# Performance work log

Hardware: AMD Instinct MI355X
Metric: run time of the kernel (lower is better)

The kernel has to match this reference:

```python
import jax, jax.numpy as jnp
import numpy as np

T, B, D, L, C, H = 100, 4096, 32, 32, 64, 128  # steps, batch, state_dim, latent, context, hidden


def setup_inputs() -> dict:
    key = jax.random.key(0)
    ks = jax.random.split(key, 32)
    def rn(k, shape, scale=0.1):
        return jax.random.normal(k, shape, dtype=jnp.float32) * scale
    return dict(
        xs=rn(ks[0], (T, B, D), 1.0),
        ts=jnp.arange(T, dtype=jnp.float32) * 0.01,
        eps0=rn(ks[1], (B, L), 1.0),
        noise=rn(ks[2], (T - 1, B, L), 1.0),
        gru_Wih=rn(ks[3], (3 * H, D)), gru_Whh=rn(ks[4], (3 * H, H)),
        gru_bih=rn(ks[5], (3 * H,)), gru_bhh=rn(ks[6], (3 * H,)),
        enc_W=rn(ks[7], (C, H)), enc_b=rn(ks[8], (C,)),
        qz0_W=rn(ks[9], (2 * L, C)), qz0_b=rn(ks[10], (2 * L,)),
        fW1=rn(ks[11], (H, L + C)), fb1=rn(ks[12], (H,)),
        fW2=rn(ks[13], (H, H)), fb2=rn(ks[14], (H,)),
        fW3=rn(ks[15], (L, H)), fb3=rn(ks[16], (L,)),
        hW1=rn(ks[17], (H, L)), hb1=rn(ks[18], (H,)),
        hW2=rn(ks[19], (H, H)), hb2=rn(ks[20], (H,)),
        hW3=rn(ks[21], (L, H)), hb3=rn(ks[22], (L,)),
        gW1=rn(ks[23], (L, H)), gb1=rn(ks[24], (L, H)),
        gW2=rn(ks[25], (L, H)), gb2=rn(ks[26], (L,)),
        projW=rn(ks[27], (D, L)), projb=rn(ks[28], (D,)),
    )


def reference(xs, ts, eps0, noise, gru_Wih, gru_Whh, gru_bih, gru_bhh,
              enc_W, enc_b, qz0_W, qz0_b,
              fW1, fb1, fW2, fb2, fW3, fb3,
              hW1, hb1, hW2, hb2, hW3, hb3,
              gW1, gb1, gW2, gb2, projW, projb):
    sp = jax.nn.softplus

    # --- Encoder: GRU (PyTorch gate order r,z,n) + Linear ---
    def gru_step(h, x):
        gi = x @ gru_Wih.T + gru_bih
        gh = h @ gru_Whh.T + gru_bhh
        ir, iz, inn = jnp.split(gi, 3, axis=-1)
        hr, hz, hn = jnp.split(gh, 3, axis=-1)
        r = jax.nn.sigmoid(ir + hr)
        z = jax.nn.sigmoid(iz + hz)
        n = jnp.tanh(inn + r * hn)
        h = (1.0 - z) * n + z * h
        return h, h

    h0 = jnp.zeros((xs.shape[1], gru_Whh.shape[1]), xs.dtype)
    _, hs = jax.lax.scan(gru_step, h0, xs)          # [T,B,H]
    ctx = hs @ enc_W.T + enc_b                      # [T,B,C]

    # --- posterior z0 ---
    qz0 = ctx[0] @ qz0_W.T + qz0_b
    mean, logstd = jnp.split(qz0, 2, axis=-1)
    z0 = mean + jnp.exp(logstd) * eps0              # [B,L]

    def f_mlp(x):  # posterior drift f_net
        return sp(sp(x @ fW1.T + fb1) @ fW2.T + fb2) @ fW3.T + fb3

    def h_mlp(y):  # prior drift h_net
        return sp(sp(y @ hW1.T + hb1) @ hW2.T + hb2) @ hW3.T + hb3

    def diag_g(y):  # batched per-dim 1->H->1 sigmoid MLPs (the g_nets loop)
        hmid = sp(y[..., None] * gW1 + gb1)          # [B,L,H]
        return jax.nn.sigmoid(jnp.sum(hmid * gW2, -1) + gb2)  # [B,L]

    dts = ts[1:] - ts[:-1]

    def sde_step(carry, inp):
        y, lq = carry
        c, dt, dW = inp
        f = f_mlp(jnp.concatenate([y, c], axis=-1))
        hdr = h_mlp(y)
        g = diag_g(y)
        u = (f - hdr) / g                            # KL path-wise term
        lq = lq + 0.5 * jnp.sum(u * u, axis=-1) * dt
        y = y + f * dt + g * jnp.sqrt(dt) * dW       # Euler-Maruyama
        return (y, lq), y

    (zT, logqp), ys = jax.lax.scan(
        sde_step, (z0, jnp.zeros(z0.shape[0], z0.dtype)), (ctx[:-1], dts, noise))
    zs = jnp.concatenate([z0[None], ys], axis=0)     # [T,B,L]
    xs_hat = zs @ projW.T + projb                    # [T,B,D]
    return xs_hat, logqp
```

## Files before the change

### kernel.cpp

```cpp
#include <hip/hip_runtime.h>


#define TT 100
#define BB 4096
#define DD 32
#define LL 32
#define CC 64
#define HH 128
#define GROW 260

typedef _Float16 h1;
typedef _Float16 h2 __attribute__((ext_vector_type(2)));
typedef _Float16 f16x8 __attribute__((ext_vector_type(8)));
typedef float f32x4 __attribute__((ext_vector_type(4)));

#define MFMA(a, b, c) __builtin_amdgcn_mfma_f32_16x16x32_f16(a, b, c, 0, 0, 0)
#define PIN(x) asm volatile("" : "+v"(x))

__device__ __forceinline__ void bar_lds() {
  __builtin_amdgcn_sched_barrier(0);
  asm volatile("s_waitcnt lgkmcnt(0)" ::: "memory");
  __builtin_amdgcn_s_barrier();
  asm volatile("" ::: "memory");
  __builtin_amdgcn_sched_barrier(0);
}

__device__ __forceinline__ float sigm(float x) {
  return __frcp_rn(1.0f + __expf(-x));
}
__device__ __forceinline__ float tanh_(float x) {
  float e = __expf(2.0f * fminf(x, 15.0f));
  return (e - 1.0f) * __frcp_rn(e + 1.0f);
}
__device__ __forceinline__ float splus(float x) {
  return __logf(1.0f + __expf(x));
}

__device__ __forceinline__ f16x8 bfrag(const float* __restrict__ W, int K,
                                       int n0, int k0, int lane) {
  const float* p = W + (size_t)(n0 + (lane & 15)) * K + k0 + ((lane >> 4) << 3);
  f16x8 r;
#pragma unroll
  for (int j = 0; j < 8; ++j) r[j] = (h1)p[j];
  return r;
}

__device__ __forceinline__ f16x8 afrag(const h1* base, int ld, int k0,
                                       int lane) {
  return *(const f16x8*)(base + (size_t)(lane & 15) * ld + k0 +
                         ((lane >> 4) << 3));
}

__global__ __launch_bounds__(320) void k_gtab(
    const float* __restrict__ gW1, const float* __restrict__ gb1,
    const float* __restrict__ gW2, const float* __restrict__ gb2,
    float* __restrict__ gtab) {
  const int l = blockIdx.x;
  const int e = threadIdx.x;
  if (e >= 257) return;
  const float yv = -12.f + (float)e * (24.f / 256.f);
  const float* w1 = gW1 + l * HH;
  const float* bb = gb1 + l * HH;
  const float* w2 = gW2 + l * HH;
  float a = 0.f;
#pragma unroll 4
  for (int h = 0; h < HH; ++h)
    a = fmaf(splus(fmaf(yv, w1[h], bb[h])), w2[h], a);
  gtab[l * GROW + e] = sigm(a + gb2[l]);
}

__global__ __launch_bounds__(512, 2) void k_gru(
    const float* __restrict__ xs, const float* __restrict__ Wih,
    const float* __restrict__ Whh, const float* __restrict__ bih,
    const float* __restrict__ bhh, const float* __restrict__ encW,
    const float* __restrict__ encb, h1* __restrict__ ctx16) {
  __shared__ alignas(16) h1 sH[2][16][136];
  __shared__ alignas(16) h1 sX[2][16][40];

  const int tid = threadIdx.x;
  const int lane = tid & 63, w = tid >> 6;
  const int b0 = blockIdx.x * 16;
  const int coln = lane & 15, row4 = (lane >> 4) << 2;

  f16x8 wIH[3], wHH[3][4], wE[4];
#pragma unroll
  for (int g = 0; g < 3; ++g) {
    wIH[g] = bfrag(Wih, DD, 128 * g + 16 * w, 0, lane);
#pragma unroll
    for (int kt = 0; kt < 4; ++kt)
      wHH[g][kt] = bfrag(Whh, HH, 128 * g + 16 * w, 32 * kt, lane);
  }
  const int m = 16 * w + coln;
  const float b_r = bih[m] + bhh[m];
  const float b_z = bih[128 + m] + bhh[128 + m];
  const float b_ni = bih[256 + m];
  const float b_nh = bhh[256 + m];
  const int ccE = (w >= 4) ? 16 * (w - 4) + coln : 0;
  const float bE = (w >= 4) ? encb[ccE] : 0.f;
  if (w >= 4) {
#pragma unroll
    for (int kt = 0; kt < 4; ++kt)
      wE[kt] = bfrag(encW, HH, 16 * (w - 4), 32 * kt, lane);
  }

  for (int i = tid; i < 16 * 136; i += 512) (&sH[0][0][0])[i] = (h1)0.0f;
  sX[0][tid >> 5][tid & 31] = (h1)xs[(size_t)b0 * DD + tid];
  float xHold = xs[(size_t)1 * BB * DD + (size_t)b0 * DD + tid];
  float hold[4] = {0.f, 0.f, 0.f, 0.f};
  __syncthreads();

  for (int t = 0; t < TT; ++t) {
    const int cur = t & 1;
    const int tf = (t + 2 < TT) ? (t + 2) : (TT - 1);
    const float xFly = xs[(size_t)tf * BB * DD + (size_t)b0 * DD + tid];

#pragma unroll
    for (int g = 0; g < 3; ++g) {
      PIN(wIH[g]);
#pragma unroll
      for (int kt = 0; kt < 4; ++kt) PIN(wHH[g][kt]);
    }
    if (w >= 4) {
#pragma unroll
      for (int kt = 0; kt < 4; ++kt) PIN(wE[kt]);
    }

    f16x8 ax = afrag(&sX[cur][0][0], 40, 0, lane);
    f32x4 aR{b_r, b_r, b_r, b_r}, aZ{b_z, b_z, b_z, b_z};
    f32x4 aNI{b_ni, b_ni, b_ni, b_ni}, aNH{b_nh, b_nh, b_nh, b_nh};
    aR = MFMA(ax, wIH[0], aR);
    aZ = MFMA(ax, wIH[1], aZ);
    aNI = MFMA(ax, wIH[2], aNI);
#pragma unroll
    for (int kt = 0; kt < 4; ++kt) {
      f16x8 ah = afrag(&sH[cur][0][0], 136, 32 * kt, lane);
      aR = MFMA(ah, wHH[0][kt], aR);
      aZ = MFMA(ah, wHH[1][kt], aZ);
      aNH = MFMA(ah, wHH[2][kt], aNH);
    }
#pragma unroll
    for (int j = 0; j < 4; ++j) {
      float rg = sigm(aR[j]);
      float zg = sigm(aZ[j]);
      float ng = tanh_(aNI[j] + rg * aNH[j]);
      float hn = (1.0f - zg) * ng + zg * hold[j];
      hold[j] = hn;
      sH[cur ^ 1][row4 + j][m] = (h1)hn;
    }
    sX[cur ^ 1][tid >> 5][tid & 31] = (h1)xHold;
    bar_lds();

    if (w >= 4) {
      f32x4 aE{bE, bE, bE, bE};
#pragma unroll
      for (int kt = 0; kt < 4; ++kt)
        aE = MFMA(afrag(&sH[cur ^ 1][0][0], 136, 32 * kt, lane), wE[kt], aE);
#pragma unroll
      for (int j = 0; j < 4; ++j)
        ctx16[((size_t)t * BB + b0 + row4 + j) * CC + ccE] = (h1)aE[j];
    }
    xHold = xFly;
  }
}

__global__ __launch_bounds__(512, 2) void k_sde(
    const float* __restrict__ ts, const float* __restrict__ eps0,
    const float* __restrict__ noise, const float* __restrict__ qz0W,
    const float* __restrict__ qz0b, const float* __restrict__ fW1,
    const float* __restrict__ fb1, const float* __restrict__ fW2,
    const float* __restrict__ fb2, const float* __restrict__ fW3,
    const float* __restrict__ fb3, const float* __restrict__ hW1,
    const float* __restrict__ hb1, const float* __restrict__ hW2,
    const float* __restrict__ hb2, const float* __restrict__ hW3,
    const float* __restrict__ hb3, const float* __restrict__ projW,
    const float* __restrict__ projb, const float* __restrict__ gtab,
    const h1* __restrict__ ctx16, float* __restrict__ out) {
  __shared__ alignas(16) h1 sC[16][72];
  __shared__ alignas(16) h1 sY16[16][40];
  __shared__ alignas(16) h1 sA1[16][136], sB1[16][136];
  __shared__ alignas(16) h1 sA2[16][136], sB2[16][136];
  __shared__ float sG[32][GROW];
  __shared__ float sDt[128], sSq[128];
  __shared__ float sTmp[16][33];

  const int tid = threadIdx.x;
  const int lane = tid & 63, w = tid >> 6;
  const int b0 = blockIdx.x * 16;
  const int coln = lane & 15, row4 = (lane >> 4) << 2;
  const bool isF = (w < 4);
  const int t2 = isF ? w : (w - 4);
  const int colA = 32 * t2 + coln, colB = colA + 16;

  f16x8 wL1a[3], wL1b[3], wL2a[4], wL2b[4], wF3[4], wH3[4], wPj;
  if (isF) {
#pragma unroll
    for (int kt = 0; kt < 3; ++kt) {
      wL1a[kt] = bfrag(fW1, 96, 32 * t2, 32 * kt, lane);
      wL1b[kt] = bfrag(fW1, 96, 32 * t2 + 16, 32 * kt, lane);
    }
#pragma unroll
    for (int kt = 0; kt < 4; ++kt) {
      wL2a[kt] = bfrag(fW2, HH, 32 * t2, 32 * kt, lane);
      wL2b[kt] = bfrag(fW2, HH, 32 * t2 + 16, 32 * kt, lane);
    }
  } else {
    wL1a[0] = bfrag(hW1, 32, 32 * t2, 0, lane);
    wL1b[0] = bfrag(hW1, 32, 32 * t2 + 16, 0, lane);
#pragma unroll
    for (int kt = 0; kt < 4; ++kt) {
      wL2a[kt] = bfrag(hW2, HH, 32 * t2, 32 * kt, lane);
      wL2b[kt] = bfrag(hW2, HH, 32 * t2 + 16, 32 * kt, lane);
    }
  }
  const float bL1a = isF ? fb1[colA] : hb1[colA];
  const float bL1b = isF ? fb1[colB] : hb1[colB];
  const float bL2a = isF ? fb2[colA] : hb2[colA];
  const float bL2b = isF ? fb2[colB] : hb2[colB];

  float bF3 = 0.f, bH3 = 0.f, bPj = 0.f;
  int cu = 0, ccp = 0, srow = 0, scol = 0;
  if (w == 4 || w == 5) {
    cu = 16 * (w - 4) + coln;
    bF3 = fb3[cu];
    bH3 = hb3[cu];
#pragma unroll
    for (int kt = 0; kt < 4; ++kt) {
      wF3[kt] = bfrag(fW3, HH, 16 * (w - 4), 32 * kt, lane);
      wH3[kt] = bfrag(hW3, HH, 16 * (w - 4), 32 * kt, lane);
    }
  } else if (w >= 6) {
    ccp = 16 * (w - 6) + coln;
    wPj = bfrag(projW, LL, 16 * (w - 6), 0, lane);
    bPj = projb[ccp];
    const int sidx = tid - 384;
    srow = sidx >> 3;
    scol = (sidx & 7) * 8;
  }

  for (int i = tid; i < 32 * GROW; i += 512) (&sG[0][0])[i] = gtab[i];
  if (tid < TT - 1) {
    float d = ts[tid + 1] - ts[tid];
    sDt[tid] = d;
    sSq[tid] = __fsqrt_rn(d);
  }
  *(h2*)&sC[tid >> 5][2 * (tid & 31)] =
      *(const h2*)(ctx16 + (size_t)(b0 + (tid >> 5)) * CC + 2 * (tid & 31));
  __syncthreads();

  {
    const int sr = tid >> 5, sc = tid & 31;
    float m0 = qz0b[sc], s0 = qz0b[32 + sc];
    const float* qm = qz0W + sc * 64;
    const float* qs = qz0W + (32 + sc) * 64;
#pragma unroll 4
    for (int k = 0; k < 64; ++k) {
      float cv = (float)sC[sr][k];
      m0 = fmaf(qm[k], cv, m0);
      s0 = fmaf(qs[k], cv, s0);
    }
    float z = fmaf(__expf(s0), eps0[(size_t)(b0 + sr) * LL + sc], m0);
    sTmp[sr][sc] = z;
    sY16[sr][sc] = (h1)z;
  }
  f16x8 cHold;
  if (w >= 6)
    cHold = *(const f16x8*)(ctx16 + ((size_t)1 * BB + b0 + srow) * CC + scol);
  float nHold[4] = {0.f, 0.f, 0.f, 0.f};
  if (w == 4 || w == 5) {
#pragma unroll
    for (int j = 0; j < 4; ++j)
      nHold[j] = noise[(size_t)(b0 + row4 + j) * LL + cu];
  }
  __syncthreads();

  float yreg[4] = {0.f, 0.f, 0.f, 0.f}, lq[4] = {0.f, 0.f, 0.f, 0.f};
  if (w == 4 || w == 5) {
#pragma unroll
    for (int j = 0; j < 4; ++j) yreg[j] = sTmp[row4 + j][cu];
  }

  f32x4 accA{bL1a, bL1a, bL1a, bL1a}, accB{bL1b, bL1b, bL1b, bL1b};
  if (isF) {
    f16x8 c0 = afrag(&sC[0][0], 72, 0, lane);
    f16x8 c1 = afrag(&sC[0][0], 72, 32, lane);
    accA = MFMA(c0, wL1a[1], accA);
    accA = MFMA(c1, wL1a[2], accA);
    accB = MFMA(c0, wL1b[1], accB);
    accB = MFMA(c1, wL1b[2], accB);
  }

  for (int t = 0; t < TT - 1; ++t) {
    f16x8 cFly;
    if (w >= 6) {
      const int tc = (t + 2 <= TT - 1) ? t + 2 : TT - 1;
      cFly = *(const f16x8*)(ctx16 + ((size_t)tc * BB + b0 + srow) * CC + scol);
    }
    float nFly[4];
    if (w == 4 || w == 5) {
      const int tn = (t + 1 < TT - 1) ? t + 1 : TT - 2;
#pragma unroll
      for (int j = 0; j < 4; ++j)
        nFly[j] = noise[((size_t)tn * BB + b0 + row4 + j) * LL + cu];
    }

    if (isF) {
#pragma unroll
      for (int kt = 0; kt < 3; ++kt) {
        PIN(wL1a[kt]);
        PIN(wL1b[kt]);
      }
    } else {
      PIN(wL1a[0]);
      PIN(wL1b[0]);
    }
#pragma unroll
    for (int kt = 0; kt < 4; ++kt) {
      PIN(wL2a[kt]);
      PIN(wL2b[kt]);
    }
    if (w == 4 || w == 5) {
#pragma unroll
      for (int kt = 0; kt < 4; ++kt) {
        PIN(wF3[kt]);
        PIN(wH3[kt]);
      }
    } else if (w >= 6) {
      PIN(wPj);
    }

    f16x8 aY = afrag(&sY16[0][0], 40, 0, lane);
    if (isF) {
      accA = MFMA(aY, wL1a[0], accA);
      accB = MFMA(aY, wL1b[0], accB);
#pragma unroll
      for (int j = 0; j < 4; ++j) {
        sA1[row4 + j][colA] = (h1)splus(accA[j]);
        sA1[row4 + j][colB] = (h1)splus(accB[j]);
      }
    } else {
      f32x4 hA{bL1a, bL1a, bL1a, bL1a}, hB{bL1b, bL1b, bL1b, bL1b};
      hA = MFMA(aY, wL1a[0], hA);
      hB = MFMA(aY, wL1b[0], hB);
#pragma unroll
      for (int j = 0; j < 4; ++j) {
        sB1[row4 + j][colA] = (h1)splus(hA[j]);
        sB1[row4 + j][colB] = (h1)splus(hB[j]);
      }
    }
    bar_lds();

    {
      const h1* src = isF ? &sA1[0][0] : &sB1[0][0];
      h1* dst = isF ? &sA2[0][0] : &sB2[0][0];
      f32x4 pA{bL2a, bL2a, bL2a, bL2a}, pB{bL2b, bL2b, bL2b, bL2b};
#pragma unroll
      for (int kt = 0; kt < 4; ++kt) {
        f16x8 a = afrag(src, 136, 32 * kt, lane);
        pA = MFMA(a, wL2a[kt], pA);
        pB = MFMA(a, wL2b[kt], pB);
      }
#pragma unroll
      for (int j = 0; j < 4; ++j) {
        dst[(size_t)(row4 + j) * 136 + colA] = (h1)splus(pA[j]);
        dst[(size_t)(row4 + j) * 136 + colB] = (h1)splus(pB[j]);
      }
    }
    if (w >= 6) {
      *(f16x8*)&sC[srow][scol] = cHold;
      cHold = cFly;
    }
    bar_lds();

    if (isF) {
      f16x8 c0 = afrag(&sC[0][0], 72, 0, lane);
      f16x8 c1 = afrag(&sC[0][0], 72, 32, lane);
      accA = f32x4{bL1a, bL1a, bL1a, bL1a};
      accB = f32x4{bL1b, bL1b, bL1b, bL1b};
      accA = MFMA(c0, wL1a[1], accA);
      accA = MFMA(c1, wL1a[2], accA);
      accB = MFMA(c0, wL1b[1], accB);
      accB = MFMA(c1, wL1b[2], accB);
    } else if (w < 6) {
      f32x4 aF{bF3, bF3, bF3, bF3}, aH{bH3, bH3, bH3, bH3};
#pragma unroll
      for (int kt = 0; kt < 4; ++kt) {
        aF = MFMA(afrag(&sA2[0][0], 136, 32 * kt, lane), wF3[kt], aF);
        aH = MFMA(afrag(&sB2[0][0], 136, 32 * kt, lane), wH3[kt], aH);
      }
      const float dtv = sDt[t], sqdt = sSq[t];
      const float* g = sG[cu];
#pragma unroll
      for (int j = 0; j < 4; ++j) {
        float p = fminf(fmaxf(fmaf(yreg[j], 32.f / 3.f, 128.f), 0.f), 255.999f);
        const int i = (int)p;
        const float fr = p - (float)i;
        const float gv = fmaf(g[i + 1] - g[i], fr, g[i]);
        const float uv = (aF[j] - aH[j]) * __frcp_rn(gv);
        lq[j] = fmaf(0.5f * uv * uv, dtv, lq[j]);
        yreg[j] = fmaf(aF[j], dtv, yreg[j]) + gv * sqdt * nHold[j];
        sY16[row4 + j][cu] = (h1)yreg[j];
      }
#pragma unroll
      for (int j = 0; j < 4; ++j) nHold[j] = nFly[j];
    } else {
      f32x4 ap{bPj, bPj, bPj, bPj};
      ap = MFMA(aY, wPj, ap);
#pragma unroll
      for (int j = 0; j < 4; ++j)
        out[((size_t)t * BB + b0 + row4 + j) * DD + ccp] = ap[j];
    }
    bar_lds();
  }

  if (w >= 6) {
    f16x8 aYf = afrag(&sY16[0][0], 40, 0, lane);
    f32x4 ap{bPj, bPj, bPj, bPj};
    ap = MFMA(aYf, wPj, ap);
#pragma unroll
    for (int j = 0; j < 4; ++j)
      out[((size_t)(TT - 1) * BB + b0 + row4 + j) * DD + ccp] = ap[j];
  }
  if (w == 4 || w == 5) {
#pragma unroll
    for (int j = 0; j < 4; ++j) sTmp[row4 + j][cu] = lq[j];
  }
  __syncthreads();
  if (tid < 16) {
    float s = 0.f;
#pragma unroll
    for (int k = 0; k < 32; ++k) s += sTmp[tid][k];
    out[(size_t)TT * BB * DD + b0 + tid] = s;
  }
}

extern "C" void kernel_launch(void* const* d_in, const int* in_sizes, int n_in,
                              void* d_out, int out_size, void* d_ws,
                              size_t ws_size, hipStream_t stream) {
  const float* xs = (const float*)d_in[0];
  const float* ts = (const float*)d_in[1];
  const float* eps0 = (const float*)d_in[2];
  const float* noise = (const float*)d_in[3];
  const float* Wih = (const float*)d_in[4];
  const float* Whh = (const float*)d_in[5];
  const float* bih = (const float*)d_in[6];
  const float* bhh = (const float*)d_in[7];
  const float* encW = (const float*)d_in[8];
  const float* encb = (const float*)d_in[9];
  const float* qz0W = (const float*)d_in[10];
  const float* qz0b = (const float*)d_in[11];
  const float* fW1 = (const float*)d_in[12];
  const float* fb1 = (const float*)d_in[13];
  const float* fW2 = (const float*)d_in[14];
  const float* fb2 = (const float*)d_in[15];
  const float* fW3 = (const float*)d_in[16];
  const float* fb3 = (const float*)d_in[17];
  const float* hW1 = (const float*)d_in[18];
  const float* hb1 = (const float*)d_in[19];
  const float* hW2 = (const float*)d_in[20];
  const float* hb2 = (const float*)d_in[21];
  const float* hW3 = (const float*)d_in[22];
  const float* hb3 = (const float*)d_in[23];
  const float* gW1 = (const float*)d_in[24];
  const float* gb1 = (const float*)d_in[25];
  const float* gW2 = (const float*)d_in[26];
  const float* gb2 = (const float*)d_in[27];
  const float* projW = (const float*)d_in[28];
  const float* projb = (const float*)d_in[29];
  float* out = (float*)d_out;
  h1* ctx16 = (h1*)d_out;
  float* gtab = (float*)d_ws;

  k_gtab<<<32, 320, 0, stream>>>(gW1, gb1, gW2, gb2, gtab);
  k_gru<<<256, 512, 0, stream>>>(xs, Wih, Whh, bih, bhh, encW, encb, ctx16);
  k_sde<<<256, 512, 0, stream>>>(ts, eps0, noise, qz0W, qz0b, fW1, fb1, fW2,
                                 fb2, fW3, fb3, hW1, hb1, hW2, hb2, hW3, hb3,
                                 projW, projb, gtab, ctx16, out);
}
```

Before: 342.4 us.

## Replicate SDE state update in every wave to drop one barrier per step

Every wave now computes the final f/h layer and the Euler-Maruyama update redundantly. It keeps the latent state in registers in a permuted column order that matches the MFMA A-fragment layout, so y no longer goes through shared memory. Context and noise are double-buffered in LDS, which removes one of the three block barriers per time step. The cost is extra MFMA and gtab-lookup work, more register pressure in all eight waves, and a permuted loading of the weight fragments.

```diff
diff --git a/kernel.cpp b/kernel.cpp
--- a/kernel.cpp
+++ b/kernel.cpp
@@ -36,12 +36,26 @@
   return __logf(1.0f + __expf(x));
 }
 
+__device__ __forceinline__ int pcol(int g, int j) {
+  return (j < 4) ? (4 * g + j) : (16 + 4 * g + (j - 4));
+}
+
 __device__ __forceinline__ f16x8 bfrag(const float* __restrict__ W, int K,
                                        int n0, int k0, int lane) {
   const float* p = W + (size_t)(n0 + (lane & 15)) * K + k0 + ((lane >> 4) << 3);
   f16x8 r;
 #pragma unroll
   for (int j = 0; j < 8; ++j) r[j] = (h1)p[j];
+  return r;
+}
+
+__device__ __forceinline__ f16x8 bfrag_p(const float* __restrict__ W, int K,
+                                         int n0, int lane) {
+  const float* p = W + (size_t)(n0 + (lane & 15)) * K;
+  const int g = lane >> 4;
+  f16x8 r;
+#pragma unroll
+  for (int j = 0; j < 8; ++j) r[j] = (h1)p[pcol(g, j)];
   return r;
 }
 
@@ -175,10 +189,10 @@
     const float* __restrict__ hb3, const float* __restrict__ projW,
     const float* __restrict__ projb, const float* __restrict__ gtab,
     const h1* __restrict__ ctx16, float* __restrict__ out) {
-  __shared__ alignas(16) h1 sC[16][72];
-  __shared__ alignas(16) h1 sY16[16][40];
+  __shared__ alignas(16) h1 sC[2][16][72];
   __shared__ alignas(16) h1 sA1[16][136], sB1[16][136];
   __shared__ alignas(16) h1 sA2[16][136], sB2[16][136];
+  __shared__ alignas(16) float sN[2][16][36];
   __shared__ float sG[32][GROW];
   __shared__ float sDt[128], sSq[128];
   __shared__ float sTmp[16][33];
@@ -187,25 +201,27 @@
   const int lane = tid & 63, w = tid >> 6;
   const int b0 = blockIdx.x * 16;
   const int coln = lane & 15, row4 = (lane >> 4) << 2;
+  const int g = lane >> 4;
   const bool isF = (w < 4);
   const int t2 = isF ? w : (w - 4);
   const int colA = 32 * t2 + coln, colB = colA + 16;
 
-  f16x8 wL1a[3], wL1b[3], wL2a[4], wL2b[4], wF3[4], wH3[4], wPj;
+  f16x8 wL1a[3], wL1b[3], wL2a[4], wL2b[4];
   if (isF) {
-#pragma unroll
-    for (int kt = 0; kt < 3; ++kt) {
-      wL1a[kt] = bfrag(fW1, 96, 32 * t2, 32 * kt, lane);
-      wL1b[kt] = bfrag(fW1, 96, 32 * t2 + 16, 32 * kt, lane);
-    }
+    wL1a[0] = bfrag_p(fW1, 96, 32 * t2, lane);
+    wL1b[0] = bfrag_p(fW1, 96, 32 * t2 + 16, lane);
+    wL1a[1] = bfrag(fW1, 96, 32 * t2, 32, lane);
+    wL1a[2] = bfrag(fW1, 96, 32 * t2, 64, lane);
+    wL1b[1] = bfrag(fW1, 96, 32 * t2 + 16, 32, lane);
+    wL1b[2] = bfrag(fW1, 96, 32 * t2 + 16, 64, lane);
 #pragma unroll
     for (int kt = 0; kt < 4; ++kt) {
       wL2a[kt] = bfrag(fW2, HH, 32 * t2, 32 * kt, lane);
       wL2b[kt] = bfrag(fW2, HH, 32 * t2 + 16, 32 * kt, lane);
     }
   } else {
-    wL1a[0] = bfrag(hW1, 32, 32 * t2, 0, lane);
-    wL1b[0] = bfrag(hW1, 32, 32 * t2 + 16, 0, lane);
+    wL1a[0] = bfrag_p(hW1, 32, 32 * t2, lane);
+    wL1b[0] = bfrag_p(hW1, 32, 32 * t2 + 16, lane);
 #pragma unroll
     for (int kt = 0; kt < 4; ++kt) {
       wL2a[kt] = bfrag(hW2, HH, 32 * t2, 32 * kt, lane);
@@ -217,20 +233,28 @@
   const float bL2a = isF ? fb2[colA] : hb2[colA];
   const float bL2b = isF ? fb2[colB] : hb2[colB];
 
-  float bF3 = 0.f, bH3 = 0.f, bPj = 0.f;
-  int cu = 0, ccp = 0, srow = 0, scol = 0;
-  if (w == 4 || w == 5) {
-    cu = 16 * (w - 4) + coln;
-    bF3 = fb3[cu];
-    bH3 = hb3[cu];
-#pragma unroll
-    for (int kt = 0; kt < 4; ++kt) {
-      wF3[kt] = bfrag(fW3, HH, 16 * (w - 4), 32 * kt, lane);
-      wH3[kt] = bfrag(hW3, HH, 16 * (w - 4), 32 * kt, lane);
-    }
-  } else if (w >= 6) {
+  f16x8 wF3[2][4], wH3[2][4];
+#pragma unroll
+  for (int kt = 0; kt < 4; ++kt) {
+    wF3[0][kt] = bfrag(fW3, HH, 0, 32 * kt, lane);
+    wF3[1][kt] = bfrag(fW3, HH, 16, 32 * kt, lane);
+    wH3[0][kt] = bfrag(hW3, HH, 0, 32 * kt, lane);
+    wH3[1][kt] = bfrag(hW3, HH, 16, 32 * kt, lane);
+  }
+  float bF3v[8], bH3v[8];
+#pragma unroll
+  for (int j = 0; j < 8; ++j) {
+    const int c = pcol(g, j);
+    bF3v[j] = fb3[c];
+    bH3v[j] = hb3[c];
+  }
+
+  f16x8 wPj;
+  float bPj = 0.f;
+  int ccp = 0, srow = 0, scol = 0;
+  if (w >= 6) {
     ccp = 16 * (w - 6) + coln;
-    wPj = bfrag(projW, LL, 16 * (w - 6), 0, lane);
+    wPj = bfrag_p(projW, LL, 16 * (w - 6), lane);
     bPj = projb[ccp];
     const int sidx = tid - 384;
     srow = sidx >> 3;
@@ -243,7 +267,7 @@
     sDt[tid] = d;
     sSq[tid] = __fsqrt_rn(d);
   }
-  *(h2*)&sC[tid >> 5][2 * (tid & 31)] =
+  *(h2*)&sC[0][tid >> 5][2 * (tid & 31)] =
       *(const h2*)(ctx16 + (size_t)(b0 + (tid >> 5)) * CC + 2 * (tid & 31));
   __syncthreads();
 
@@ -254,54 +278,35 @@
     const float* qs = qz0W + (32 + sc) * 64;
 #pragma unroll 4
     for (int k = 0; k < 64; ++k) {
-      float cv = (float)sC[sr][k];
+      float cv = (float)sC[0][sr][k];
       m0 = fmaf(qm[k], cv, m0);
       s0 = fmaf(qs[k], cv, s0);
     }
-    float z = fmaf(__expf(s0), eps0[(size_t)(b0 + sr) * LL + sc], m0);
-    sTmp[sr][sc] = z;
-    sY16[sr][sc] = (h1)z;
+    sTmp[sr][sc] = fmaf(__expf(s0), eps0[(size_t)(b0 + sr) * LL + sc], m0);
+  }
+  __syncthreads();
+
+  float yreg[8], lq[8];
+#pragma unroll
+  for (int j = 0; j < 8; ++j) {
+    yreg[j] = sTmp[coln][pcol(g, j)];
+    lq[j] = 0.f;
   }
   f16x8 cHold;
   if (w >= 6)
     cHold = *(const f16x8*)(ctx16 + ((size_t)1 * BB + b0 + srow) * CC + scol);
-  float nHold[4] = {0.f, 0.f, 0.f, 0.f};
-  if (w == 4 || w == 5) {
-#pragma unroll
-    for (int j = 0; j < 4; ++j)
-      nHold[j] = noise[(size_t)(b0 + row4 + j) * LL + cu];
-  }
+  float nHold = noise[(size_t)(b0 + (tid >> 5)) * LL + (tid & 31)];
   __syncthreads();
 
-  float yreg[4] = {0.f, 0.f, 0.f, 0.f}, lq[4] = {0.f, 0.f, 0.f, 0.f};
-  if (w == 4 || w == 5) {
-#pragma unroll
-    for (int j = 0; j < 4; ++j) yreg[j] = sTmp[row4 + j][cu];
-  }
-
-  f32x4 accA{bL1a, bL1a, bL1a, bL1a}, accB{bL1b, bL1b, bL1b, bL1b};
-  if (isF) {
-    f16x8 c0 = afrag(&sC[0][0], 72, 0, lane);
-    f16x8 c1 = afrag(&sC[0][0], 72, 32, lane);
-    accA = MFMA(c0, wL1a[1], accA);
-    accA = MFMA(c1, wL1a[2], accA);
-    accB = MFMA(c0, wL1b[1], accB);
-    accB = MFMA(c1, wL1b[2], accB);
-  }
-
   for (int t = 0; t < TT - 1; ++t) {
+    const int cb = t & 1;
+    const int tn = (t + 1 < TT - 1) ? (t + 1) : (TT - 2);
+    const float nFly = noise[((size_t)tn * BB + b0 + (tid >> 5)) * LL + (tid & 31)];
     f16x8 cFly;
     if (w >= 6) {
       const int tc = (t + 2 <= TT - 1) ? t + 2 : TT - 1;
       cFly = *(const f16x8*)(ctx16 + ((size_t)tc * BB + b0 + srow) * CC + scol);
     }
-    float nFly[4];
-    if (w == 4 || w == 5) {
-      const int tn = (t + 1 < TT - 1) ? t + 1 : TT - 2;
-#pragma unroll
-      for (int j = 0; j < 4; ++j)
-        nFly[j] = noise[((size_t)tn * BB + b0 + row4 + j) * LL + cu];
-    }
 
     if (isF) {
 #pragma unroll
@@ -317,19 +322,66 @@
     for (int kt = 0; kt < 4; ++kt) {
       PIN(wL2a[kt]);
       PIN(wL2b[kt]);
-    }
-    if (w == 4 || w == 5) {
+      PIN(wF3[0][kt]);
+      PIN(wF3[1][kt]);
+      PIN(wH3[0][kt]);
+      PIN(wH3[1][kt]);
+    }
+    if (w >= 6) PIN(wPj);
+
+    if (t > 0) {
+      f32x4 f0{bF3v[0], bF3v[1], bF3v[2], bF3v[3]};
+      f32x4 f1{bF3v[4], bF3v[5], bF3v[6], bF3v[7]};
+      f32x4 h0{bH3v[0], bH3v[1], bH3v[2], bH3v[3]};
+      f32x4 hh1{bH3v[4], bH3v[5], bH3v[6], bH3v[7]};
 #pragma unroll
       for (int kt = 0; kt < 4; ++kt) {
-        PIN(wF3[kt]);
-        PIN(wH3[kt]);
-      }
-    } else if (w >= 6) {
-      PIN(wPj);
-    }
-
-    f16x8 aY = afrag(&sY16[0][0], 40, 0, lane);
+        f16x8 a2 = afrag(&sA2[0][0], 136, 32 * kt, lane);
+        f16x8 b2 = afrag(&sB2[0][0], 136, 32 * kt, lane);
+        f0 = MFMA(wF3[0][kt], a2, f0);
+        f1 = MFMA(wF3[1][kt], a2, f1);
+        h0 = MFMA(wH3[0][kt], b2, h0);
+        hh1 = MFMA(wH3[1][kt], b2, hh1);
+      }
+      const float dtv = sDt[t - 1], sqdt = sSq[t - 1];
+      const f32x4 nA = *(const f32x4*)&sN[cb ^ 1][coln][4 * g];
+      const f32x4 nB = *(const f32x4*)&sN[cb ^ 1][coln][16 + 4 * g];
+#pragma unroll
+      for (int j = 0; j < 4; ++j) {
+        {
+          const float* gr = sG[4 * g + j];
+          float p = fminf(fmaxf(fmaf(yreg[j], 32.f / 3.f, 128.f), 0.f), 255.999f);
+          const int i = (int)p;
+          const float fr = p - (float)i;
+          const float gv = fmaf(gr[i + 1] - gr[i], fr, gr[i]);
+          const float uv = (f0[j] - h0[j]) * __frcp_rn(gv);
+          lq[j] = fmaf(0.5f * uv * uv, dtv, lq[j]);
+          yreg[j] = fmaf(f0[j], dtv, yreg[j]) + gv * sqdt * nA[j];
+        }
+        {
+          const float* gr = sG[16 + 4 * g + j];
+          float p =
+              fminf(fmaxf(fmaf(yreg[4 + j], 32.f / 3.f, 128.f), 0.f), 255.999f);
+          const int i = (int)p;
+          const float fr = p - (float)i;
+          const float gv = fmaf(gr[i + 1] - gr[i], fr, gr[i]);
+          const float uv = (f1[j] - hh1[j]) * __frcp_rn(gv);
+          lq[4 + j] = fmaf(0.5f * uv * uv, dtv, lq[4 + j]);
+          yreg[4 + j] = fmaf(f1[j], dtv, yreg[4 + j]) + gv * sqdt * nB[j];
+        }
+      }
+    }
+    f16x8 aY;
+#pragma unroll
+    for (int j = 0; j < 8; ++j) aY[j] = (h1)yreg[j];
     if (isF) {
+      f16x8 c0 = afrag(&sC[cb][0][0], 72, 0, lane);
+      f16x8 c1 = afrag(&sC[cb][0][0], 72, 32, lane);
+      f32x4 accA{bL1a, bL1a, bL1a, bL1a}, accB{bL1b, bL1b, bL1b, bL1b};
+      accA = MFMA(c0, wL1a[1], accA);
+      accA = MFMA(c1, wL1a[2], accA);
+      accB = MFMA(c0, wL1b[1], accB);
+      accB = MFMA(c1, wL1b[2], accB);
       accA = MFMA(aY, wL1a[0], accA);
       accB = MFMA(aY, wL1b[0], accB);
 #pragma unroll
@@ -365,72 +417,77 @@
         dst[(size_t)(row4 + j) * 136 + colB] = (h1)splus(pB[j]);
       }
     }
+    sN[cb][tid >> 5][tid & 31] = nHold;
+    nHold = nFly;
     if (w >= 6) {
-      *(f16x8*)&sC[srow][scol] = cHold;
+      *(f16x8*)&sC[cb ^ 1][srow][scol] = cHold;
       cHold = cFly;
+      f32x4 ap{bPj, bPj, bPj, bPj};
+      ap = MFMA(aY, wPj, ap);
+#pragma unroll
+      for (int j = 0; j < 4; ++j)
+        out[((size_t)t * BB + b0 + row4 + j) * DD + ccp] = ap[j];
     }
     bar_lds();
-
-    if (isF) {
-      f16x8 c0 = afrag(&sC[0][0], 72, 0, lane);
-      f16x8 c1 = afrag(&sC[0][0], 72, 32, lane);
-      accA = f32x4{bL1a, bL1a, bL1a, bL1a};
-      accB = f32x4{bL1b, bL1b, bL1b, bL1b};
-      accA = MFMA(c0, wL1a[1], accA);
-      accA = MFMA(c1, wL1a[2], accA);
-      accB = MFMA(c0, wL1b[1], accB);
-      accB = MFMA(c1, wL1b[2], accB);
-    } else if (w < 6) {
-      f32x4 aF{bF3, bF3, bF3, bF3}, aH{bH3, bH3, bH3, bH3};
-#pragma unroll
-      for (int kt = 0; kt < 4; ++kt) {
-        aF = MFMA(afrag(&sA2[0][0], 136, 32 * kt, lane), wF3[kt], aF);
-        aH = MFMA(afrag(&sB2[0][0], 136, 32 * kt, lane), wH3[kt], aH);
-      }
-      const float dtv = sDt[t], sqdt = sSq[t];
-      const float* g = sG[cu];
-#pragma unroll
-      for (int j = 0; j < 4; ++j) {
+  }
+
+  {
+    f32x4 f0{bF3v[0], bF3v[1], bF3v[2], bF3v[3]};
+    f32x4 f1{bF3v[4], bF3v[5], bF3v[6], bF3v[7]};
+    f32x4 h0{bH3v[0], bH3v[1], bH3v[2], bH3v[3]};
+    f32x4 hh1{bH3v[4], bH3v[5], bH3v[6], bH3v[7]};
+#pragma unroll
+    for (int kt = 0; kt < 4; ++kt) {
+      f16x8 a2 = afrag(&sA2[0][0], 136, 32 * kt, lane);
+      f16x8 b2 = afrag(&sB2[0][0], 136, 32 * kt, lane);
+      f0 = MFMA(wF3[0][kt], a2, f0);
+      f1 = MFMA(wF3[1][kt], a2, f1);
+      h0 = MFMA(wH3[0][kt], b2, h0);
+      hh1 = MFMA(wH3[1][kt], b2, hh1);
+    }
+    const float dtv = sDt[TT - 2], sqdt = sSq[TT - 2];
+    const f32x4 nA = *(const f32x4*)&sN[(TT - 2) & 1][coln][4 * g];
+    const f32x4 nB = *(const f32x4*)&sN[(TT - 2) & 1][coln][16 + 4 * g];
+#pragma unroll
+    for (int j = 0; j < 4; ++j) {
+      {
+        const float* gr = sG[4 * g + j];
         float p = fminf(fmaxf(fmaf(yreg[j], 32.f / 3.f, 128.f), 0.f), 255.999f);
         const int i = (int)p;
         const float fr = p - (float)i;
-        const float gv = fmaf(g[i + 1] - g[i], fr, g[i]);
-        const float uv = (aF[j] - aH[j]) * __frcp_rn(gv);
+        const float gv = fmaf(gr[i + 1] - gr[i], fr, gr[i]);
+        const float uv = (f0[j] - h0[j]) * __frcp_rn(gv);
         lq[j] = fmaf(0.5f * uv * uv, dtv, lq[j]);
-        yreg[j] = fmaf(aF[j], dtv, yreg[j]) + gv * sqdt * nHold[j];
-        sY16[row4 + j][cu] = (h1)yreg[j];
-      }
-#pragma unroll
-      for (int j = 0; j < 4; ++j) nHold[j] = nFly[j];
-    } else {
-      f32x4 ap{bPj, bPj, bPj, bPj};
-      ap = MFMA(aY, wPj, ap);
-#pragma unroll
-      for (int j = 0; j < 4; ++j)
-        out[((size_t)t * BB + b0 + row4 + j) * DD + ccp] = ap[j];
-    }
-    bar_lds();
-  }
-
+        yreg[j] = fmaf(f0[j], dtv, yreg[j]) + gv * sqdt * nA[j];
+      }
+      {
+        const float* gr = sG[16 + 4 * g + j];
+        float p =
+            fminf(fmaxf(fmaf(yreg[4 + j], 32.f / 3.f, 128.f), 0.f), 255.999f);
+        const int i = (int)p;
+        const float fr = p - (float)i;
+        const float gv = fmaf(gr[i + 1] - gr[i], fr, gr[i]);
+        const float uv = (f1[j] - hh1[j]) * __frcp_rn(gv);
+        lq[4 + j] = fmaf(0.5f * uv * uv, dtv, lq[4 + j]);
+        yreg[4 + j] = fmaf(f1[j], dtv, yreg[4 + j]) + gv * sqdt * nB[j];
+      }
+    }
+  }
   if (w >= 6) {
-    f16x8 aYf = afrag(&sY16[0][0], 40, 0, lane);
+    f16x8 aYf;
+#pragma unroll
+    for (int j = 0; j < 8; ++j) aYf[j] = (h1)yreg[j];
     f32x4 ap{bPj, bPj, bPj, bPj};
     ap = MFMA(aYf, wPj, ap);
 #pragma unroll
     for (int j = 0; j < 4; ++j)
       out[((size_t)(TT - 1) * BB + b0 + row4 + j) * DD + ccp] = ap[j];
   }
-  if (w == 4 || w == 5) {
-#pragma unroll
-    for (int j = 0; j < 4; ++j) sTmp[row4 + j][cu] = lq[j];
-  }
-  __syncthreads();
-  if (tid < 16) {
-    float s = 0.f;
-#pragma unroll
-    for (int k = 0; k < 32; ++k) s += sTmp[tid][k];
-    out[(size_t)TT * BB * DD + b0 + tid] = s;
-  }
+  float s8 = ((lq[0] + lq[1]) + (lq[2] + lq[3])) +
+             ((lq[4] + lq[5]) + (lq[6] + lq[7]));
+  s8 += __shfl_xor(s8, 16);
+  s8 += __shfl_xor(s8, 32);
+  if (w == 0 && lane < 16) out[(size_t)TT * BB * DD + b0 + lane] = s8;
 }
 
 extern "C" void kernel_launch(void* const* d_in, const int* in_sizes, int n_in,
```

New measurement: 427.4 us. 24.8% more time.
